# Performance work log

Measured on AMD Instinct MI355X. Metric: run time of the kernel, lower is better.

The kernel has to match this reference:

```python
import jax, jax.numpy as jnp
import numpy as np

G, N, E = 64, 1000, 8192          # graphs, nodes/graph, edges/graph
F_IN, C, H, HID, NCLS = 128, 128, 4, 256, 2
EPS = 1e-5


def _gcn(x, src, dst, W, b):
    # GCNConv: symmetric normalization with self-loops, sum aggregation.
    h = x @ W                                              # [N, C]
    deg = jax.ops.segment_sum(jnp.ones(E, h.dtype), dst, num_segments=N) + 1.0
    dinv = jax.lax.rsqrt(deg)                              # deg^{-1/2}
    msg = h[src] * (dinv[src] * dinv[dst])[:, None]        # [E, C] gather
    out = jax.ops.segment_sum(msg, dst, num_segments=N)    # scatter-add
    out = out + h * (dinv * dinv)[:, None]                 # self-loop term
    return out + b


def _layernorm(y, g, b):
    mu = y.mean(-1, keepdims=True)
    var = ((y - mu) ** 2).mean(-1, keepdims=True)
    return (y - mu) * jax.lax.rsqrt(var + EPS) * g + b


def setup_inputs() -> dict:
    key = jax.random.key(0)
    ks = jax.random.split(key, 12)
    rn = lambda k, s: jax.random.normal(k, s, jnp.float32) * 0.05
    return dict(
        x=jax.random.normal(ks[0], (G, N, F_IN), jnp.float32),
        edge_index=jax.random.randint(ks[1], (G, 2, E), 0, N),
        W0=rn(ks[2], (F_IN, C)), b0=jnp.zeros((C,), jnp.float32),
        W1=rn(ks[3], (C, C)), b1=jnp.zeros((C,), jnp.float32),
        in_w=rn(ks[4], (3 * C, C)), in_b=jnp.zeros((3 * C,), jnp.float32),
        out_w=rn(ks[5], (C, C)), out_b=jnp.zeros((C,), jnp.float32),
        ln2_g=jnp.ones((C,), jnp.float32), ln2_b=jnp.zeros((C,), jnp.float32),
        mw1=rn(ks[6], (C, HID)), mb1=jnp.zeros((HID,), jnp.float32),
        mw2=rn(ks[7], (HID, C)), mb2=jnp.zeros((C,), jnp.float32),
        lw=rn(ks[8], (C, NCLS)), lb=jnp.zeros((NCLS,), jnp.float32),
    )


def reference(x, edge_index, W0, b0, W1, b1, in_w, in_b, out_w, out_b,
              ln2_g, ln2_b, mw1, mb1, mw2, mb2, lw, lb):
    src, dst = edge_index[:, 0, :], edge_index[:, 1, :]
    conv = jax.vmap(_gcn, in_axes=(0, 0, 0, None, None))
    h = jnp.tanh(conv(x, src, dst, W0, b0))   # [G, N, C]
    h = jnp.tanh(conv(h, src, dst, W1, b1))
    g = h.sum(axis=1)                          # SumAggregation -> [G, C]

    # MultiheadAttention, unbatched: sequence of G graph embeddings
    qkv = g @ in_w.T + in_b
    q, k, v = jnp.split(qkv, 3, axis=-1)
    d = C // H
    qh, kh, vh = (t.reshape(G, H, d) for t in (q, k, v))
    attn = jax.nn.softmax(jnp.einsum('qhd,khd->hqk', qh, kh) * (d ** -0.5), axis=-1)
    o = jnp.einsum('hqk,khd->qhd', attn, vh).reshape(G, C) @ out_w.T + out_b

    x_attend = o                               # dropout = identity (eval)
    # NOTE: original computes layer_norm1(x_attend) but immediately overwrites it.
    mlp = jnp.maximum(x_attend @ mw1 + mb1, 0.0) @ mw2 + mb2
    y = _layernorm(x_attend + mlp, ln2_g, ln2_b)
    node_repr = jnp.maximum(y, 0.0).sum(axis=0)  # [C]
    return node_repr @ lw + lb                   # [NCLS]
```

## Files before the change

kernel.cpp:

```cpp
#include <hip/hip_runtime.h>
#include <math.h>

#define Gn 64
#define Nn 1000
#define En 8192
#define Cc 128
#define HIDn 256
#define EPSf 1e-5f

typedef __attribute__((ext_vector_type(8))) short bh8;
typedef __attribute__((ext_vector_type(4))) float fx4;

__device__ __forceinline__ unsigned short f2bf(float f) {
    unsigned u = __float_as_uint(f);
    u += 0x7fffu + ((u >> 16) & 1u);
    return (unsigned short)(u >> 16);
}
__device__ __forceinline__ float bflo(unsigned u) { return __uint_as_float(u << 16); }
__device__ __forceinline__ float bfhi(unsigned u) { return __uint_as_float(u & 0xffff0000u); }

__global__ __launch_bounds__(256) void k_pre(const int* __restrict__ ei,
                                             const float* __restrict__ W0, const float* __restrict__ W1,
                                             int4* __restrict__ ninfo, int2* __restrict__ epair,
                                             float* __restrict__ pooled, float* __restrict__ repr,
                                             int* __restrict__ ctr,
                                             unsigned short* __restrict__ Wt0g,
                                             unsigned short* __restrict__ Wt1g)
{
    __shared__ int   curs[1024];
    __shared__ float dinv_s[1024];
    __shared__ int   wsum[4];
    __shared__ __align__(16) short Wls[128][136];
    int t = threadIdx.x;

    if (blockIdx.x >= 64) {
        const float* Wsrc = (blockIdx.x == 64) ? W0 : W1;
        unsigned short* Wdst = (blockIdx.x == 64) ? Wt0g : Wt1g;
        for (int idx = t; idx < 16384; idx += 256) {
            int kI = idx >> 7, n = idx & 127;
            Wls[n][kI] = (short)f2bf(Wsrc[idx]);
        }
        __syncthreads();
        for (int idx = t; idx < 2048; idx += 256) {
            int n = idx >> 4, kc = idx & 15;
            bh8 v = *(const bh8*)&Wls[n][kc * 8];
            *(bh8*)(Wdst + (size_t)idx * 8) = v;
        }
        return;
    }

    int g = blockIdx.x;
    const int* srcp = ei + (size_t)g * 2 * En;
    const int* dstp = srcp + En;
    int lane = t & 63, wv = t >> 6;

    #pragma unroll
    for (int j = 0; j < 4; ++j) curs[t * 4 + j] = 0;
    __syncthreads();
    for (int e = t; e < En; e += 256) atomicAdd(&curs[dstp[e]], 1);
    __syncthreads();

    int base = t * 4;
    int d0 = curs[base], d1 = curs[base + 1], d2 = curs[base + 2], d3 = curs[base + 3];
    int s = d0 + d1 + d2 + d3;
    int v = s;
    #pragma unroll
    for (int off = 1; off <= 32; off <<= 1) {
        int u = __shfl_up(v, off);
        if (lane >= off) v += u;
    }
    if (lane == 63) wsum[wv] = v;
    __syncthreads();
    int woff = 0;
    #pragma unroll
    for (int w = 0; w < 4; ++w) if (w < wv) woff += wsum[w];
    int e0 = woff + v - s;
    int e1 = e0 + d0, e2 = e1 + d1, e3 = e2 + d2;
    float dv0 = rsqrtf((float)d0 + 1.f), dv1 = rsqrtf((float)d1 + 1.f);
    float dv2 = rsqrtf((float)d2 + 1.f), dv3 = rsqrtf((float)d3 + 1.f);
    curs[base] = e0; curs[base + 1] = e1; curs[base + 2] = e2; curs[base + 3] = e3;
    dinv_s[base] = dv0; dinv_s[base + 1] = dv1; dinv_s[base + 2] = dv2; dinv_s[base + 3] = dv3;
    if (base < Nn)     ninfo[g * Nn + base]     = make_int4(e0, d0, __float_as_int(dv0 * dv0), 0);
    if (base + 1 < Nn) ninfo[g * Nn + base + 1] = make_int4(e1, d1, __float_as_int(dv1 * dv1), 0);
    if (base + 2 < Nn) ninfo[g * Nn + base + 2] = make_int4(e2, d2, __float_as_int(dv2 * dv2), 0);
    if (base + 3 < Nn) ninfo[g * Nn + base + 3] = make_int4(e3, d3, __float_as_int(dv3 * dv3), 0);
    __syncthreads();

    for (int e = t; e < En; e += 256) {
        int dd = dstp[e], ss = srcp[e];
        int p = atomicAdd(&curs[dd], 1);
        float w = dinv_s[ss] * dinv_s[dd];
        epair[(size_t)g * En + p] = make_int2(ss, __float_as_int(w));
    }
    if (t < Cc) pooled[g * Cc + t] = 0.f;
    if (g == 0 && t < Cc) repr[t] = 0.f;
    if (g == 0 && t == 0) *ctr = 0;
}

template<int INBF>
__global__ __launch_bounds__(256) void k_gemm(const void* __restrict__ Xin,
                                              const unsigned short* __restrict__ Wtg,
                                              unsigned short* __restrict__ Hout)
{
    __shared__ __align__(16) short Wt[128][136];
    int b = blockIdx.x;
    int xcd = b & 7, gg = (b >> 3) & 7, rblk = b >> 6;
    int g = xcd + 8 * gg;
    int t = threadIdx.x;
    for (int idx = t; idx < 2048; idx += 256) {
        int n = idx >> 4, kc = idx & 15;
        bh8 v = *(const bh8*)(Wtg + (size_t)idx * 8);
        *(bh8*)&Wt[n][kc * 8] = v;
    }
    __syncthreads();

    int wave = t >> 6, l = t & 63;
    int lr = l & 15, lg = l >> 4;
    const float* Xf = (const float*)Xin + (size_t)g * Nn * Cc;
    const short* Xh = (const short*)Xin + (size_t)g * Nn * Cc;
    unsigned short* Hg = Hout + (size_t)g * Nn * Cc;

    int rbase = rblk * 64 + wave * 16;
    int r = rbase + lr;
    bool ok = r < Nn;
    bh8 af[4];
    if (INBF) {
        #pragma unroll
        for (int ks = 0; ks < 4; ++ks) {
            if (ok) af[ks] = *(const bh8*)(Xh + (size_t)r * Cc + ks * 32 + lg * 8);
            else    af[ks] = bh8{0, 0, 0, 0, 0, 0, 0, 0};
        }
    } else {
        #pragma unroll
        for (int ks = 0; ks < 4; ++ks) {
            if (ok) {
                const float* xp = Xf + (size_t)r * Cc + ks * 32 + lg * 8;
                fx4 a0 = *(const fx4*)xp;
                fx4 a1 = *(const fx4*)(xp + 4);
                bh8 av;
                av[0] = (short)f2bf(a0[0]); av[1] = (short)f2bf(a0[1]);
                av[2] = (short)f2bf(a0[2]); av[3] = (short)f2bf(a0[3]);
                av[4] = (short)f2bf(a1[0]); av[5] = (short)f2bf(a1[1]);
                av[6] = (short)f2bf(a1[2]); av[7] = (short)f2bf(a1[3]);
                af[ks] = av;
            } else af[ks] = bh8{0, 0, 0, 0, 0, 0, 0, 0};
        }
    }
    fx4 acc[8];
    #pragma unroll
    for (int ct = 0; ct < 8; ++ct) acc[ct] = fx4{0.f, 0.f, 0.f, 0.f};
    #pragma unroll
    for (int ks = 0; ks < 4; ++ks) {
        #pragma unroll
        for (int ct = 0; ct < 8; ++ct) {
            bh8 bfr = *(const bh8*)(&Wt[ct * 16 + lr][ks * 32 + lg * 8]);
            acc[ct] = __builtin_amdgcn_mfma_f32_16x16x32_bf16(af[ks], bfr, acc[ct], 0, 0, 0);
        }
    }
    #pragma unroll
    for (int ct = 0; ct < 8; ++ct) {
        #pragma unroll
        for (int rg = 0; rg < 4; ++rg) {
            int row = rbase + lg * 4 + rg;
            if (row < Nn) Hg[(size_t)row * Cc + ct * 16 + lr] = f2bf(acc[ct][rg]);
        }
    }
}

template<int POOL>
__global__ __launch_bounds__(256) void k_combine(const unsigned* __restrict__ Hb, const int2* __restrict__ epair,
                                                 const int4* __restrict__ ninfo, const float* __restrict__ bias,
                                                 unsigned* __restrict__ Tout, float* __restrict__ pooled)
{
    int b = blockIdx.x;
    int xcd = b & 7, j = b >> 3;
    int g = xcd + 8 * (j & 7);
    int blk = j >> 3;
    int wave = threadIdx.x >> 6, lane = threadIdx.x & 63;
    const unsigned* Hg = Hb + (size_t)g * Nn * 64;
    const int2* epg = epair + (size_t)g * En;
    const int4* nig = ninfo + (size_t)g * Nn;
    float2 bb = *(const float2*)(bias + lane * 2);
    float px = 0.f, py = 0.f;
    for (int n = blk * 4 + wave; n < Nn; n += 128) {
        int4 ni = nig[n];
        int st = ni.x, dc = ni.y;
        float sw = __int_as_float(ni.z);
        unsigned hv = Hg[n * 64 + lane];
        float a0x = bflo(hv) * sw + bb.x, a0y = bfhi(hv) * sw + bb.y;
        float a1x = 0.f, a1y = 0.f, a2x = 0.f, a2y = 0.f, a3x = 0.f, a3y = 0.f;
        int e = 0;
        for (; e + 4 <= dc; e += 4) {
            int2 p0 = epg[st + e];
            int2 p1 = epg[st + e + 1];
            int2 p2 = epg[st + e + 2];
            int2 p3 = epg[st + e + 3];
            unsigned r0 = Hg[(size_t)p0.x * 64 + lane];
            unsigned r1 = Hg[(size_t)p1.x * 64 + lane];
            unsigned r2 = Hg[(size_t)p2.x * 64 + lane];
            unsigned r3 = Hg[(size_t)p3.x * 64 + lane];
            float w0 = __int_as_float(p0.y), w1 = __int_as_float(p1.y);
            float w2 = __int_as_float(p2.y), w3 = __int_as_float(p3.y);
            a0x = fmaf(bflo(r0), w0, a0x); a0y = fmaf(bfhi(r0), w0, a0y);
            a1x = fmaf(bflo(r1), w1, a1x); a1y = fmaf(bfhi(r1), w1, a1y);
            a2x = fmaf(bflo(r2), w2, a2x); a2y = fmaf(bfhi(r2), w2, a2y);
            a3x = fmaf(bflo(r3), w3, a3x); a3y = fmaf(bfhi(r3), w3, a3y);
        }
        for (; e < dc; ++e) {
            int2 p0 = epg[st + e];
            unsigned r0 = Hg[(size_t)p0.x * 64 + lane];
            float w0 = __int_as_float(p0.y);
            a0x = fmaf(bflo(r0), w0, a0x); a0y = fmaf(bfhi(r0), w0, a0y);
        }
        float ax = (a0x + a1x) + (a2x + a3x);
        float ay = (a0y + a1y) + (a2y + a3y);
        float tx = tanhf(ax), ty = tanhf(ay);
        if (POOL) { px += tx; py += ty; }
        else Tout[(size_t)(g * Nn + n) * 64 + lane] = ((unsigned)f2bf(ty) << 16) | (unsigned)f2bf(tx);
    }
    if (POOL) {
        atomicAdd(&pooled[g * Cc + lane * 2], px);
        atomicAdd(&pooled[g * Cc + lane * 2 + 1], py);
    }
}

__global__ __launch_bounds__(1024) void k_qkv(const float* __restrict__ pooled, const float* __restrict__ in_w,
                                              const float* __restrict__ in_b, float* __restrict__ qkvb)
{
    int t = threadIdx.x, lane = t & 63, wv = t >> 6;
    int c = blockIdx.x * 16 + wv;
    const float* wr = in_w + c * Cc;
    float w0 = wr[lane], w1 = wr[64 + lane];
    float bias = in_b[c];
    for (int i = 0; i < Gn; ++i) {
        float p = fmaf(pooled[i * Cc + lane], w0, pooled[i * Cc + 64 + lane] * w1);
        #pragma unroll
        for (int off2 = 32; off2 > 0; off2 >>= 1) p += __shfl_xor(p, off2);
        if (lane == 0) qkvb[i * 384 + c] = p + bias;
    }
}

__global__ __launch_bounds__(1024) void k_attn(const float* __restrict__ qkvb, float* __restrict__ ob)
{
    __shared__ float q[64][33], kk[64][33], v[64][33];
    __shared__ float S[64][64];
    int h = blockIdx.x, t = threadIdx.x;

    for (int idx = t; idx < 2048; idx += 1024) {
        int i = idx >> 5, cc = idx & 31;
        q[i][cc]  = qkvb[i * 384 + h * 32 + cc];
        kk[i][cc] = qkvb[i * 384 + 128 + h * 32 + cc];
        v[i][cc]  = qkvb[i * 384 + 256 + h * 32 + cc];
    }
    __syncthreads();

    for (int idx = t; idx < 4096; idx += 1024) {
        int i = idx >> 6, jj = idx & 63;
        float acc = 0.f;
        #pragma unroll
        for (int d2 = 0; d2 < 32; ++d2) acc = fmaf(q[i][d2], kk[jj][d2], acc);
        S[i][jj] = acc * 0.17677669529663687f;
    }
    __syncthreads();

    int lane = t & 63, w = t >> 6;
    for (int r = w; r < 64; r += 16) {
        float val = S[r][lane];
        float m = val;
        #pragma unroll
        for (int off = 32; off > 0; off >>= 1) m = fmaxf(m, __shfl_xor(m, off));
        float e2 = expf(val - m);
        float ssum = e2;
        #pragma unroll
        for (int off = 32; off > 0; off >>= 1) ssum += __shfl_xor(ssum, off);
        S[r][lane] = e2 / ssum;
    }
    __syncthreads();

    for (int idx = t; idx < 2048; idx += 1024) {
        int i = idx >> 5, d2 = idx & 31;
        float acc = 0.f;
        #pragma unroll 4
        for (int k2 = 0; k2 < 64; ++k2) acc = fmaf(S[i][k2], v[k2][d2], acc);
        ob[i * Cc + h * 32 + d2] = acc;
    }
}

__global__ __launch_bounds__(512) void k_tailfinal(const float* __restrict__ ob, const float* __restrict__ out_w,
                                                   const float* __restrict__ out_b, const float* __restrict__ mw1,
                                                   const float* __restrict__ mb1, const float* __restrict__ mw2,
                                                   const float* __restrict__ mb2, const float* __restrict__ ln2g,
                                                   const float* __restrict__ ln2b, const float* __restrict__ lw,
                                                   const float* __restrict__ lb, float* __restrict__ repr,
                                                   int* __restrict__ ctr, float* __restrict__ out)
{
    __shared__ float sob[128];
    __shared__ float sxatt[128];
    __shared__ float sm1p[2][256];
    __shared__ float sm1[256];
    __shared__ float sp2[4][128];
    __shared__ float yb[128];
    __shared__ int slast;
    int g = blockIdx.x;
    int t = threadIdx.x, lane = t & 63, wv = t >> 6;

    if (t < 128) sob[t] = ob[(size_t)g * Cc + t];
    __syncthreads();

    {
        float o0 = sob[lane], o1 = sob[64 + lane];
        for (int c = wv; c < Cc; c += 8) {
            const float* wr = out_w + c * Cc;
            float p = fmaf(o0, wr[lane], o1 * wr[64 + lane]);
            #pragma unroll
            for (int off = 32; off > 0; off >>= 1) p += __shfl_xor(p, off);
            if (lane == 0) sxatt[c] = p + out_b[c];
        }
    }
    __syncthreads();

    {
        int jc = t & 255, half = t >> 8;
        int k0b = half * 64;
        float a[8];
        #pragma unroll
        for (int u = 0; u < 8; ++u) a[u] = 0.f;
        for (int k0 = k0b; k0 < k0b + 64; k0 += 8) {
            #pragma unroll
            for (int u = 0; u < 8; ++u)
                a[u] = fmaf(sxatt[k0 + u], mw1[(size_t)(k0 + u) * HIDn + jc], a[u]);
        }
        sm1p[half][jc] = ((a[0] + a[1]) + (a[2] + a[3])) + ((a[4] + a[5]) + (a[6] + a[7]));
        __syncthreads();
        if (t < 256) sm1[t] = fmaxf(sm1p[0][t] + sm1p[1][t] + mb1[t], 0.f);
    }
    __syncthreads();

    {
        int c = t & 127, q = t >> 7;
        int j0b = q * 64;
        float a[8];
        #pragma unroll
        for (int u = 0; u < 8; ++u) a[u] = 0.f;
        for (int j0 = j0b; j0 < j0b + 64; j0 += 8) {
            #pragma unroll
            for (int u = 0; u < 8; ++u)
                a[u] = fmaf(sm1[j0 + u], mw2[(size_t)(j0 + u) * Cc + c], a[u]);
        }
        sp2[q][c] = ((a[0] + a[1]) + (a[2] + a[3])) + ((a[4] + a[5]) + (a[6] + a[7]));
        __syncthreads();
        if (t < 128) yb[t] = sxatt[t] + (sp2[0][t] + sp2[1][t]) + (sp2[2][t] + sp2[3][t]) + mb2[t];
    }
    __syncthreads();

    if (t < 64) {
        float v0 = yb[lane], v1 = yb[64 + lane];
        float s = v0 + v1;
        #pragma unroll
        for (int off = 32; off > 0; off >>= 1) s += __shfl_xor(s, off);
        float mu = s * (1.f / 128.f);
        float d0 = v0 - mu, d1 = v1 - mu;
        float vv = d0 * d0 + d1 * d1;
        #pragma unroll
        for (int off = 32; off > 0; off >>= 1) vv += __shfl_xor(vv, off);
        float rstd = rsqrtf(vv * (1.f / 128.f) + EPSf);
        float z0 = fmaxf(d0 * rstd * ln2g[lane] + ln2b[lane], 0.f);
        float z1 = fmaxf(d1 * rstd * ln2g[64 + lane] + ln2b[64 + lane], 0.f);
        atomicAdd(&repr[lane], z0);
        atomicAdd(&repr[64 + lane], z1);
    }

    __threadfence();
    __syncthreads();
    if (t == 0) slast = atomicAdd(ctr, 1);
    __syncthreads();
    if (slast == 63) {
        __threadfence();
        __shared__ float r0s[128], r1s[128];
        if (t < 128) {
            float r = __hip_atomic_load(&repr[t], __ATOMIC_RELAXED, __HIP_MEMORY_SCOPE_AGENT);
            r0s[t] = r * lw[t * 2 + 0];
            r1s[t] = r * lw[t * 2 + 1];
        }
        __syncthreads();
        for (int s2 = 64; s2 > 0; s2 >>= 1) {
            if (t < s2) { r0s[t] += r0s[t + s2]; r1s[t] += r1s[t + s2]; }
            __syncthreads();
        }
        if (t == 0) { out[0] = r0s[0] + lb[0]; out[1] = r1s[0] + lb[1]; }
    }
}

extern "C" void kernel_launch(void* const* d_in, const int* in_sizes, int n_in,
                              void* d_out, int out_size, void* d_ws, size_t ws_size,
                              hipStream_t stream)
{
    const float* x     = (const float*)d_in[0];
    const int*   ei    = (const int*)d_in[1];
    const float* W0    = (const float*)d_in[2];
    const float* b0    = (const float*)d_in[3];
    const float* W1    = (const float*)d_in[4];
    const float* b1    = (const float*)d_in[5];
    const float* in_w  = (const float*)d_in[6];
    const float* in_b  = (const float*)d_in[7];
    const float* out_w = (const float*)d_in[8];
    const float* out_b = (const float*)d_in[9];
    const float* ln2g  = (const float*)d_in[10];
    const float* ln2b  = (const float*)d_in[11];
    const float* mw1   = (const float*)d_in[12];
    const float* mb1   = (const float*)d_in[13];
    const float* mw2   = (const float*)d_in[14];
    const float* mb2   = (const float*)d_in[15];
    const float* lw    = (const float*)d_in[16];
    const float* lb    = (const float*)d_in[17];
    float* out = (float*)d_out;
    (void)in_sizes; (void)n_in; (void)out_size; (void)ws_size;

    char* ws = (char*)d_ws;
    size_t off = 0;
    auto carve = [&](size_t bytes) { size_t o = off; off += (bytes + 255) & ~(size_t)255; return o; };
    size_t o_ni    = carve((size_t)Gn * Nn * 16);
    size_t o_ep    = carve((size_t)Gn * En * 8);
    size_t o_pool  = carve((size_t)Gn * Cc * 4);
    size_t o_qkv   = carve((size_t)Gn * 384 * 4);
    size_t o_ob    = carve((size_t)Gn * Cc * 4);
    size_t o_repr  = carve((size_t)Cc * 4);
    size_t o_ctr   = carve(256);
    size_t o_W0t   = carve((size_t)Cc * Cc * 2);
    size_t o_W1t   = carve((size_t)Cc * Cc * 2);
    size_t o_H     = carve((size_t)Gn * Nn * Cc * 2);
    size_t o_T     = carve((size_t)Gn * Nn * Cc * 2);

    int4*  ninfo  = (int4*)(ws + o_ni);
    int2*  epair  = (int2*)(ws + o_ep);
    float* pooled = (float*)(ws + o_pool);
    float* qkvb   = (float*)(ws + o_qkv);
    float* ob     = (float*)(ws + o_ob);
    float* repr   = (float*)(ws + o_repr);
    int*   ctr    = (int*)(ws + o_ctr);
    unsigned short* Wt0g = (unsigned short*)(ws + o_W0t);
    unsigned short* Wt1g = (unsigned short*)(ws + o_W1t);
    unsigned short* H  = (unsigned short*)(ws + o_H);
    unsigned short* T  = (unsigned short*)(ws + o_T);

    k_pre<<<66, 256, 0, stream>>>(ei, W0, W1, ninfo, epair, pooled, repr, ctr, Wt0g, Wt1g);
    k_gemm<0><<<1024, 256, 0, stream>>>(x, Wt0g, H);
    k_combine<0><<<2048, 256, 0, stream>>>((const unsigned*)H, epair, ninfo, b0, (unsigned*)T, nullptr);
    k_gemm<1><<<1024, 256, 0, stream>>>(T, Wt1g, H);
    k_combine<1><<<2048, 256, 0, stream>>>((const unsigned*)H, epair, ninfo, b1, nullptr, pooled);
    k_qkv<<<24, 1024, 0, stream>>>(pooled, in_w, in_b, qkvb);
    k_attn<<<4, 1024, 0, stream>>>(qkvb, ob);
    k_tailfinal<<<64, 512, 0, stream>>>(ob, out_w, out_b, mw1, mb1, mw2, mb2, ln2g, ln2b,
                                        lw, lb, repr, ctr, out);
}
```

Before: 170.4 us.

## Fuse preprocessing with first GEMM and merge attention head kernels via grid barriers

```diff
diff --git a/kernel.cpp b/kernel.cpp
--- a/kernel.cpp
+++ b/kernel.cpp
@@ -19,88 +19,140 @@
 __device__ __forceinline__ float bflo(unsigned u) { return __uint_as_float(u << 16); }
 __device__ __forceinline__ float bfhi(unsigned u) { return __uint_as_float(u & 0xffff0000u); }
 
-__global__ __launch_bounds__(256) void k_pre(const int* __restrict__ ei,
+__global__ __launch_bounds__(256) void k_g0p(const int* __restrict__ ei, const float* __restrict__ X,
                                              const float* __restrict__ W0, const float* __restrict__ W1,
                                              int4* __restrict__ ninfo, int2* __restrict__ epair,
                                              float* __restrict__ pooled, float* __restrict__ repr,
-                                             int* __restrict__ ctr,
-                                             unsigned short* __restrict__ Wt0g,
-                                             unsigned short* __restrict__ Wt1g)
+                                             int* __restrict__ bars,
+                                             unsigned short* __restrict__ Wt1g,
+                                             unsigned short* __restrict__ Hout)
 {
-    __shared__ int   curs[1024];
-    __shared__ float dinv_s[1024];
-    __shared__ int   wsum[4];
-    __shared__ __align__(16) short Wls[128][136];
+    __shared__ __align__(16) short Wt[128][136];
+    __shared__ int wsum[4];
     int t = threadIdx.x;
-
-    if (blockIdx.x >= 64) {
-        const float* Wsrc = (blockIdx.x == 64) ? W0 : W1;
-        unsigned short* Wdst = (blockIdx.x == 64) ? Wt0g : Wt1g;
+    int b = blockIdx.x;
+
+    if (b < 64) {
+        int* curs = (int*)&Wt[0][0];
+        float* dinv_s = (float*)((char*)&Wt[0][0] + 4096);
+        int g = b;
+        const int* srcp = ei + (size_t)g * 2 * En;
+        const int* dstp = srcp + En;
+        int lane = t & 63, wv = t >> 6;
+
+        #pragma unroll
+        for (int j = 0; j < 4; ++j) curs[t * 4 + j] = 0;
+        __syncthreads();
+        for (int e = t; e < En; e += 256) atomicAdd(&curs[dstp[e]], 1);
+        __syncthreads();
+
+        int base = t * 4;
+        int d0 = curs[base], d1 = curs[base + 1], d2 = curs[base + 2], d3 = curs[base + 3];
+        int s = d0 + d1 + d2 + d3;
+        int v = s;
+        #pragma unroll
+        for (int off = 1; off <= 32; off <<= 1) {
+            int u = __shfl_up(v, off);
+            if (lane >= off) v += u;
+        }
+        if (lane == 63) wsum[wv] = v;
+        __syncthreads();
+        int woff = 0;
+        #pragma unroll
+        for (int w = 0; w < 4; ++w) if (w < wv) woff += wsum[w];
+        int e0 = woff + v - s;
+        int e1 = e0 + d0, e2 = e1 + d1, e3 = e2 + d2;
+        float dv0 = rsqrtf((float)d0 + 1.f), dv1 = rsqrtf((float)d1 + 1.f);
+        float dv2 = rsqrtf((float)d2 + 1.f), dv3 = rsqrtf((float)d3 + 1.f);
+        curs[base] = e0; curs[base + 1] = e1; curs[base + 2] = e2; curs[base + 3] = e3;
+        dinv_s[base] = dv0; dinv_s[base + 1] = dv1; dinv_s[base + 2] = dv2; dinv_s[base + 3] = dv3;
+        if (base < Nn)     ninfo[g * Nn + base]     = make_int4(e0, d0, __float_as_int(dv0 * dv0), 0);
+        if (base + 1 < Nn) ninfo[g * Nn + base + 1] = make_int4(e1, d1, __float_as_int(dv1 * dv1), 0);
+        if (base + 2 < Nn) ninfo[g * Nn + base + 2] = make_int4(e2, d2, __float_as_int(dv2 * dv2), 0);
+        if (base + 3 < Nn) ninfo[g * Nn + base + 3] = make_int4(e3, d3, __float_as_int(dv3 * dv3), 0);
+        __syncthreads();
+
+        for (int e = t; e < En; e += 256) {
+            int dd = dstp[e], ss = srcp[e];
+            int p = atomicAdd(&curs[dd], 1);
+            float w = dinv_s[ss] * dinv_s[dd];
+            epair[(size_t)g * En + p] = make_int2(ss, __float_as_int(w));
+        }
+        if (t < Cc) pooled[g * Cc + t] = 0.f;
+        if (g == 0 && t < Cc) repr[t] = 0.f;
+        if (g == 0 && t < 4) bars[t] = 0;
+        return;
+    }
+
+    if (b == 1088) {
         for (int idx = t; idx < 16384; idx += 256) {
             int kI = idx >> 7, n = idx & 127;
-            Wls[n][kI] = (short)f2bf(Wsrc[idx]);
+            Wt[n][kI] = (short)f2bf(W1[idx]);
         }
         __syncthreads();
         for (int idx = t; idx < 2048; idx += 256) {
             int n = idx >> 4, kc = idx & 15;
-            bh8 v = *(const bh8*)&Wls[n][kc * 8];
-            *(bh8*)(Wdst + (size_t)idx * 8) = v;
+            *(bh8*)(Wt1g + (size_t)idx * 8) = *(const bh8*)&Wt[n][kc * 8];
         }
         return;
     }
 
-    int g = blockIdx.x;
-    const int* srcp = ei + (size_t)g * 2 * En;
-    const int* dstp = srcp + En;
-    int lane = t & 63, wv = t >> 6;
-
-    #pragma unroll
-    for (int j = 0; j < 4; ++j) curs[t * 4 + j] = 0;
-    __syncthreads();
-    for (int e = t; e < En; e += 256) atomicAdd(&curs[dstp[e]], 1);
-    __syncthreads();
-
-    int base = t * 4;
-    int d0 = curs[base], d1 = curs[base + 1], d2 = curs[base + 2], d3 = curs[base + 3];
-    int s = d0 + d1 + d2 + d3;
-    int v = s;
-    #pragma unroll
-    for (int off = 1; off <= 32; off <<= 1) {
-        int u = __shfl_up(v, off);
-        if (lane >= off) v += u;
-    }
-    if (lane == 63) wsum[wv] = v;
-    __syncthreads();
-    int woff = 0;
-    #pragma unroll
-    for (int w = 0; w < 4; ++w) if (w < wv) woff += wsum[w];
-    int e0 = woff + v - s;
-    int e1 = e0 + d0, e2 = e1 + d1, e3 = e2 + d2;
-    float dv0 = rsqrtf((float)d0 + 1.f), dv1 = rsqrtf((float)d1 + 1.f);
-    float dv2 = rsqrtf((float)d2 + 1.f), dv3 = rsqrtf((float)d3 + 1.f);
-    curs[base] = e0; curs[base + 1] = e1; curs[base + 2] = e2; curs[base + 3] = e3;
-    dinv_s[base] = dv0; dinv_s[base + 1] = dv1; dinv_s[base + 2] = dv2; dinv_s[base + 3] = dv3;
-    if (base < Nn)     ninfo[g * Nn + base]     = make_int4(e0, d0, __float_as_int(dv0 * dv0), 0);
-    if (base + 1 < Nn) ninfo[g * Nn + base + 1] = make_int4(e1, d1, __float_as_int(dv1 * dv1), 0);
-    if (base + 2 < Nn) ninfo[g * Nn + base + 2] = make_int4(e2, d2, __float_as_int(dv2 * dv2), 0);
-    if (base + 3 < Nn) ninfo[g * Nn + base + 3] = make_int4(e3, d3, __float_as_int(dv3 * dv3), 0);
-    __syncthreads();
-
-    for (int e = t; e < En; e += 256) {
-        int dd = dstp[e], ss = srcp[e];
-        int p = atomicAdd(&curs[dd], 1);
-        float w = dinv_s[ss] * dinv_s[dd];
-        epair[(size_t)g * En + p] = make_int2(ss, __float_as_int(w));
-    }
-    if (t < Cc) pooled[g * Cc + t] = 0.f;
-    if (g == 0 && t < Cc) repr[t] = 0.f;
-    if (g == 0 && t == 0) *ctr = 0;
-}
-
-template<int INBF>
-__global__ __launch_bounds__(256) void k_gemm(const void* __restrict__ Xin,
-                                              const unsigned short* __restrict__ Wtg,
-                                              unsigned short* __restrict__ Hout)
+    int bb = b - 64;
+    int xcd = bb & 7, gg = (bb >> 3) & 7, rblk = bb >> 6;
+    int g = xcd + 8 * gg;
+    for (int idx = t; idx < 16384; idx += 256) {
+        int kI = idx >> 7, n = idx & 127;
+        Wt[n][kI] = (short)f2bf(W0[idx]);
+    }
+    __syncthreads();
+
+    int wave = t >> 6, l = t & 63;
+    int lr = l & 15, lg = l >> 4;
+    const float* Xf = X + (size_t)g * Nn * Cc;
+    unsigned short* Hg = Hout + (size_t)g * Nn * Cc;
+
+    int rbase = rblk * 64 + wave * 16;
+    int r = rbase + lr;
+    bool ok = r < Nn;
+    bh8 af[4];
+    #pragma unroll
+    for (int ks = 0; ks < 4; ++ks) {
+        if (ok) {
+            const float* xp = Xf + (size_t)r * Cc + ks * 32 + lg * 8;
+            fx4 a0 = *(const fx4*)xp;
+            fx4 a1 = *(const fx4*)(xp + 4);
+            bh8 av;
+            av[0] = (short)f2bf(a0[0]); av[1] = (short)f2bf(a0[1]);
+            av[2] = (short)f2bf(a0[2]); av[3] = (short)f2bf(a0[3]);
+            av[4] = (short)f2bf(a1[0]); av[5] = (short)f2bf(a1[1]);
+            av[6] = (short)f2bf(a1[2]); av[7] = (short)f2bf(a1[3]);
+            af[ks] = av;
+        } else af[ks] = bh8{0, 0, 0, 0, 0, 0, 0, 0};
+    }
+    fx4 acc[8];
+    #pragma unroll
+    for (int ct = 0; ct < 8; ++ct) acc[ct] = fx4{0.f, 0.f, 0.f, 0.f};
+    #pragma unroll
+    for (int ks = 0; ks < 4; ++ks) {
+        #pragma unroll
+        for (int ct = 0; ct < 8; ++ct) {
+            bh8 bfr = *(const bh8*)(&Wt[ct * 16 + lr][ks * 32 + lg * 8]);
+            acc[ct] = __builtin_amdgcn_mfma_f32_16x16x32_bf16(af[ks], bfr, acc[ct], 0, 0, 0);
+        }
+    }
+    #pragma unroll
+    for (int ct = 0; ct < 8; ++ct) {
+        #pragma unroll
+        for (int rg = 0; rg < 4; ++rg) {
+            int row = rbase + lg * 4 + rg;
+            if (row < Nn) Hg[(size_t)row * Cc + ct * 16 + lr] = f2bf(acc[ct][rg]);
+        }
+    }
+}
+
+__global__ __launch_bounds__(256) void k_gemm1(const unsigned short* __restrict__ Xh,
+                                               const unsigned short* __restrict__ Wtg,
+                                               unsigned short* __restrict__ Hout)
 {
     __shared__ __align__(16) short Wt[128][136];
     int b = blockIdx.x;
@@ -116,35 +168,17 @@
 
     int wave = t >> 6, l = t & 63;
     int lr = l & 15, lg = l >> 4;
-    const float* Xf = (const float*)Xin + (size_t)g * Nn * Cc;
-    const short* Xh = (const short*)Xin + (size_t)g * Nn * Cc;
+    const short* Xg = (const short*)Xh + (size_t)g * Nn * Cc;
     unsigned short* Hg = Hout + (size_t)g * Nn * Cc;
 
     int rbase = rblk * 64 + wave * 16;
     int r = rbase + lr;
     bool ok = r < Nn;
     bh8 af[4];
-    if (INBF) {
-        #pragma unroll
-        for (int ks = 0; ks < 4; ++ks) {
-            if (ok) af[ks] = *(const bh8*)(Xh + (size_t)r * Cc + ks * 32 + lg * 8);
-            else    af[ks] = bh8{0, 0, 0, 0, 0, 0, 0, 0};
-        }
-    } else {
-        #pragma unroll
-        for (int ks = 0; ks < 4; ++ks) {
-            if (ok) {
-                const float* xp = Xf + (size_t)r * Cc + ks * 32 + lg * 8;
-                fx4 a0 = *(const fx4*)xp;
-                fx4 a1 = *(const fx4*)(xp + 4);
-                bh8 av;
-                av[0] = (short)f2bf(a0[0]); av[1] = (short)f2bf(a0[1]);
-                av[2] = (short)f2bf(a0[2]); av[3] = (short)f2bf(a0[3]);
-                av[4] = (short)f2bf(a1[0]); av[5] = (short)f2bf(a1[1]);
-                av[6] = (short)f2bf(a1[2]); av[7] = (short)f2bf(a1[3]);
-                af[ks] = av;
-            } else af[ks] = bh8{0, 0, 0, 0, 0, 0, 0, 0};
-        }
+    #pragma unroll
+    for (int ks = 0; ks < 4; ++ks) {
+        if (ok) af[ks] = *(const bh8*)(Xg + (size_t)r * Cc + ks * 32 + lg * 8);
+        else    af[ks] = bh8{0, 0, 0, 0, 0, 0, 0, 0};
     }
     fx4 acc[8];
     #pragma unroll
@@ -186,7 +220,7 @@
         int4 ni = nig[n];
         int st = ni.x, dc = ni.y;
         float sw = __int_as_float(ni.z);
-        unsigned hv = Hg[n * 64 + lane];
+        unsigned hv = Hg[(size_t)n * 64 + lane];
         float a0x = bflo(hv) * sw + bb.x, a0y = bfhi(hv) * sw + bb.y;
         float a1x = 0.f, a1y = 0.f, a2x = 0.f, a2y = 0.f, a3x = 0.f, a3y = 0.f;
         int e = 0;
@@ -224,87 +258,94 @@
     }
 }
 
-__global__ __launch_bounds__(1024) void k_qkv(const float* __restrict__ pooled, const float* __restrict__ in_w,
-                                              const float* __restrict__ in_b, float* __restrict__ qkvb)
+__global__ __launch_bounds__(512) void k_head(const float* __restrict__ pooled, const float* __restrict__ in_w,
+                                              const float* __restrict__ in_b, const float* __restrict__ out_w,
+                                              const float* __restrict__ out_b, const float* __restrict__ mw1,
+                                              const float* __restrict__ mb1, const float* __restrict__ mw2,
+                                              const float* __restrict__ mb2, const float* __restrict__ ln2g,
+                                              const float* __restrict__ ln2b, const float* __restrict__ lw,
+                                              const float* __restrict__ lb, float* __restrict__ qkvb,
+                                              float* __restrict__ ob, float* __restrict__ repr,
+                                              int* __restrict__ bars, float* __restrict__ out)
 {
-    int t = threadIdx.x, lane = t & 63, wv = t >> 6;
-    int c = blockIdx.x * 16 + wv;
-    const float* wr = in_w + c * Cc;
-    float w0 = wr[lane], w1 = wr[64 + lane];
-    float bias = in_b[c];
-    for (int i = 0; i < Gn; ++i) {
-        float p = fmaf(pooled[i * Cc + lane], w0, pooled[i * Cc + 64 + lane] * w1);
-        #pragma unroll
-        for (int off2 = 32; off2 > 0; off2 >>= 1) p += __shfl_xor(p, off2);
-        if (lane == 0) qkvb[i * 384 + c] = p + bias;
-    }
-}
-
-__global__ __launch_bounds__(1024) void k_attn(const float* __restrict__ qkvb, float* __restrict__ ob)
-{
-    __shared__ float q[64][33], kk[64][33], v[64][33];
+    __shared__ float spool[128];
+    __shared__ float q[64][33], kk[64][33], vv[64][33];
     __shared__ float S[64][64];
-    int h = blockIdx.x, t = threadIdx.x;
-
-    for (int idx = t; idx < 2048; idx += 1024) {
-        int i = idx >> 5, cc = idx & 31;
-        q[i][cc]  = qkvb[i * 384 + h * 32 + cc];
-        kk[i][cc] = qkvb[i * 384 + 128 + h * 32 + cc];
-        v[i][cc]  = qkvb[i * 384 + 256 + h * 32 + cc];
-    }
-    __syncthreads();
-
-    for (int idx = t; idx < 4096; idx += 1024) {
-        int i = idx >> 6, jj = idx & 63;
-        float acc = 0.f;
-        #pragma unroll
-        for (int d2 = 0; d2 < 32; ++d2) acc = fmaf(q[i][d2], kk[jj][d2], acc);
-        S[i][jj] = acc * 0.17677669529663687f;
-    }
-    __syncthreads();
-
-    int lane = t & 63, w = t >> 6;
-    for (int r = w; r < 64; r += 16) {
-        float val = S[r][lane];
-        float m = val;
-        #pragma unroll
-        for (int off = 32; off > 0; off >>= 1) m = fmaxf(m, __shfl_xor(m, off));
-        float e2 = expf(val - m);
-        float ssum = e2;
-        #pragma unroll
-        for (int off = 32; off > 0; off >>= 1) ssum += __shfl_xor(ssum, off);
-        S[r][lane] = e2 / ssum;
-    }
-    __syncthreads();
-
-    for (int idx = t; idx < 2048; idx += 1024) {
-        int i = idx >> 5, d2 = idx & 31;
-        float acc = 0.f;
-        #pragma unroll 4
-        for (int k2 = 0; k2 < 64; ++k2) acc = fmaf(S[i][k2], v[k2][d2], acc);
-        ob[i * Cc + h * 32 + d2] = acc;
-    }
-}
-
-__global__ __launch_bounds__(512) void k_tailfinal(const float* __restrict__ ob, const float* __restrict__ out_w,
-                                                   const float* __restrict__ out_b, const float* __restrict__ mw1,
-                                                   const float* __restrict__ mb1, const float* __restrict__ mw2,
-                                                   const float* __restrict__ mb2, const float* __restrict__ ln2g,
-                                                   const float* __restrict__ ln2b, const float* __restrict__ lw,
-                                                   const float* __restrict__ lb, float* __restrict__ repr,
-                                                   int* __restrict__ ctr, float* __restrict__ out)
-{
-    __shared__ float sob[128];
-    __shared__ float sxatt[128];
-    __shared__ float sm1p[2][256];
-    __shared__ float sm1[256];
-    __shared__ float sp2[4][128];
-    __shared__ float yb[128];
+    __shared__ float sob[128], sxatt[128], sm1p[2][256], sm1[256], sp2[4][128], yb[128];
     __shared__ int slast;
-    int g = blockIdx.x;
-    int t = threadIdx.x, lane = t & 63, wv = t >> 6;
-
-    if (t < 128) sob[t] = ob[(size_t)g * Cc + t];
+    int g = blockIdx.x, t = threadIdx.x, lane = t & 63, wv = t >> 6;
+
+    if (t < 128) spool[t] = pooled[g * Cc + t];
+    __syncthreads();
+    {
+        float p0 = spool[lane], p1 = spool[64 + lane];
+        for (int c = wv; c < 384; c += 8) {
+            const float* wr = in_w + c * Cc;
+            float p = fmaf(p0, wr[lane], p1 * wr[64 + lane]);
+            #pragma unroll
+            for (int off = 32; off > 0; off >>= 1) p += __shfl_xor(p, off);
+            if (lane == 0)
+                __hip_atomic_store(&qkvb[g * 384 + c], p + in_b[c],
+                                   __ATOMIC_RELAXED, __HIP_MEMORY_SCOPE_AGENT);
+        }
+    }
+    __syncthreads();
+    if (t == 0) {
+        __hip_atomic_fetch_add(&bars[0], 1, __ATOMIC_RELEASE, __HIP_MEMORY_SCOPE_AGENT);
+        while (__hip_atomic_load(&bars[0], __ATOMIC_ACQUIRE, __HIP_MEMORY_SCOPE_AGENT) < Gn) {}
+    }
+    __syncthreads();
+
+    if (g < 4) {
+        int h = g;
+        for (int idx = t; idx < 2048; idx += 512) {
+            int i = idx >> 5, cc = idx & 31;
+            q[i][cc]  = __hip_atomic_load(&qkvb[i * 384 + h * 32 + cc],
+                                          __ATOMIC_RELAXED, __HIP_MEMORY_SCOPE_AGENT);
+            kk[i][cc] = __hip_atomic_load(&qkvb[i * 384 + 128 + h * 32 + cc],
+                                          __ATOMIC_RELAXED, __HIP_MEMORY_SCOPE_AGENT);
+            vv[i][cc] = __hip_atomic_load(&qkvb[i * 384 + 256 + h * 32 + cc],
+                                          __ATOMIC_RELAXED, __HIP_MEMORY_SCOPE_AGENT);
+        }
+        __syncthreads();
+        for (int idx = t; idx < 4096; idx += 512) {
+            int i = idx >> 6, jj = idx & 63;
+            float acc = 0.f;
+            #pragma unroll
+            for (int d2 = 0; d2 < 32; ++d2) acc = fmaf(q[i][d2], kk[jj][d2], acc);
+            S[i][jj] = acc * 0.17677669529663687f;
+        }
+        __syncthreads();
+        for (int r = wv; r < 64; r += 8) {
+            float val = S[r][lane];
+            float m = val;
+            #pragma unroll
+            for (int off = 32; off > 0; off >>= 1) m = fmaxf(m, __shfl_xor(m, off));
+            float e2 = expf(val - m);
+            float ssum = e2;
+            #pragma unroll
+            for (int off = 32; off > 0; off >>= 1) ssum += __shfl_xor(ssum, off);
+            S[r][lane] = e2 / ssum;
+        }
+        __syncthreads();
+        for (int idx = t; idx < 2048; idx += 512) {
+            int i = idx >> 5, d2 = idx & 31;
+            float acc = 0.f;
+            #pragma unroll 4
+            for (int k2 = 0; k2 < 64; ++k2) acc = fmaf(S[i][k2], vv[k2][d2], acc);
+            __hip_atomic_store(&ob[i * Cc + h * 32 + d2], acc,
+                               __ATOMIC_RELAXED, __HIP_MEMORY_SCOPE_AGENT);
+        }
+    }
+    __syncthreads();
+    if (t == 0) {
+        __hip_atomic_fetch_add(&bars[1], 1, __ATOMIC_RELEASE, __HIP_MEMORY_SCOPE_AGENT);
+        while (__hip_atomic_load(&bars[1], __ATOMIC_ACQUIRE, __HIP_MEMORY_SCOPE_AGENT) < Gn) {}
+    }
+    __syncthreads();
+
+    if (t < 128) sob[t] = __hip_atomic_load(&ob[(size_t)g * Cc + t],
+                                            __ATOMIC_RELAXED, __HIP_MEMORY_SCOPE_AGENT);
     __syncthreads();
 
     {
@@ -337,8 +378,8 @@
     __syncthreads();
 
     {
-        int c = t & 127, q = t >> 7;
-        int j0b = q * 64;
+        int c = t & 127, qq = t >> 7;
+        int j0b = qq * 64;
         float a[8];
         #pragma unroll
         for (int u = 0; u < 8; ++u) a[u] = 0.f;
@@ -347,7 +388,7 @@
             for (int u = 0; u < 8; ++u)
                 a[u] = fmaf(sm1[j0 + u], mw2[(size_t)(j0 + u) * Cc + c], a[u]);
         }
-        sp2[q][c] = ((a[0] + a[1]) + (a[2] + a[3])) + ((a[4] + a[5]) + (a[6] + a[7]));
+        sp2[qq][c] = ((a[0] + a[1]) + (a[2] + a[3])) + ((a[4] + a[5]) + (a[6] + a[7]));
         __syncthreads();
         if (t < 128) yb[t] = sxatt[t] + (sp2[0][t] + sp2[1][t]) + (sp2[2][t] + sp2[3][t]) + mb2[t];
     }
@@ -360,10 +401,10 @@
         for (int off = 32; off > 0; off >>= 1) s += __shfl_xor(s, off);
         float mu = s * (1.f / 128.f);
         float d0 = v0 - mu, d1 = v1 - mu;
-        float vv = d0 * d0 + d1 * d1;
-        #pragma unroll
-        for (int off = 32; off > 0; off >>= 1) vv += __shfl_xor(vv, off);
-        float rstd = rsqrtf(vv * (1.f / 128.f) + EPSf);
+        float vvr = d0 * d0 + d1 * d1;
+        #pragma unroll
+        for (int off = 32; off > 0; off >>= 1) vvr += __shfl_xor(vvr, off);
+        float rstd = rsqrtf(vvr * (1.f / 128.f) + EPSf);
         float z0 = fmaxf(d0 * rstd * ln2g[lane] + ln2b[lane], 0.f);
         float z1 = fmaxf(d1 * rstd * ln2g[64 + lane] + ln2b[64 + lane], 0.f);
         atomicAdd(&repr[lane], z0);
@@ -372,7 +413,7 @@
 
     __threadfence();
     __syncthreads();
-    if (t == 0) slast = atomicAdd(ctr, 1);
+    if (t == 0) slast = atomicAdd(&bars[2], 1);
     __syncthreads();
     if (slast == 63) {
         __threadfence();
@@ -425,8 +466,7 @@
     size_t o_qkv   = carve((size_t)Gn * 384 * 4);
     size_t o_ob    = carve((size_t)Gn * Cc * 4);
     size_t o_repr  = carve((size_t)Cc * 4);
-    size_t o_ctr   = carve(256);
-    size_t o_W0t   = carve((size_t)Cc * Cc * 2);
+    size_t o_bars  = carve(256);
     size_t o_W1t   = carve((size_t)Cc * Cc * 2);
     size_t o_H     = carve((size_t)Gn * Nn * Cc * 2);
     size_t o_T     = carve((size_t)Gn * Nn * Cc * 2);
@@ -437,19 +477,15 @@
     float* qkvb   = (float*)(ws + o_qkv);
     float* ob     = (float*)(ws + o_ob);
     float* repr   = (float*)(ws + o_repr);
-    int*   ctr    = (int*)(ws + o_ctr);
-    unsigned short* Wt0g = (unsigned short*)(ws + o_W0t);
+    int*   bars   = (int*)(ws + o_bars);
     unsigned short* Wt1g = (unsigned short*)(ws + o_W1t);
     unsigned short* H  = (unsigned short*)(ws + o_H);
     unsigned short* T  = (unsigned short*)(ws + o_T);
 
-    k_pre<<<66, 256, 0, stream>>>(ei, W0, W1, ninfo, epair, pooled, repr, ctr, Wt0g, Wt1g);
-    k_gemm<0><<<1024, 256, 0, stream>>>(x, Wt0g, H);
+    k_g0p<<<1089, 256, 0, stream>>>(ei, x, W0, W1, ninfo, epair, pooled, repr, bars, Wt1g, H);
     k_combine<0><<<2048, 256, 0, stream>>>((const unsigned*)H, epair, ninfo, b0, (unsigned*)T, nullptr);
-    k_gemm<1><<<1024, 256, 0, stream>>>(T, Wt1g, H);
+    k_gemm1<<<1024, 256, 0, stream>>>(T, Wt1g, H);
     k_combine<1><<<2048, 256, 0, stream>>>((const unsigned*)H, epair, ninfo, b1, nullptr, pooled);
-    k_qkv<<<24, 1024, 0, stream>>>(pooled, in_w, in_b, qkvb);
-    k_attn<<<4, 1024, 0, stream>>>(qkvb, ob);
-    k_tailfinal<<<64, 512, 0, stream>>>(ob, out_w, out_b, mw1, mb1, mw2, mb2, ln2g, ln2b,
-                                        lw, lb, repr, ctr, out);
-}
+    k_head<<<64, 512, 0, stream>>>(pooled, in_w, in_b, out_w, out_b, mw1, mb1, mw2, mb2,
+                                   ln2g, ln2b, lw, lb, qkvb, ob, repr, bars, out);
+}
```

After: 176.3 us. 1.03x slower.

## Fuse graph preprocessing and first-layer GEMM into a single kernel launch

Applied to the files above, without the earlier changes.

```diff
diff --git a/kernel.cpp b/kernel.cpp
--- a/kernel.cpp
+++ b/kernel.cpp
@@ -19,88 +19,140 @@
 __device__ __forceinline__ float bflo(unsigned u) { return __uint_as_float(u << 16); }
 __device__ __forceinline__ float bfhi(unsigned u) { return __uint_as_float(u & 0xffff0000u); }
 
-__global__ __launch_bounds__(256) void k_pre(const int* __restrict__ ei,
+__global__ __launch_bounds__(256) void k_g0p(const int* __restrict__ ei, const float* __restrict__ X,
                                              const float* __restrict__ W0, const float* __restrict__ W1,
                                              int4* __restrict__ ninfo, int2* __restrict__ epair,
                                              float* __restrict__ pooled, float* __restrict__ repr,
-                                             int* __restrict__ ctr,
-                                             unsigned short* __restrict__ Wt0g,
-                                             unsigned short* __restrict__ Wt1g)
-{
-    __shared__ int   curs[1024];
-    __shared__ float dinv_s[1024];
-    __shared__ int   wsum[4];
-    __shared__ __align__(16) short Wls[128][136];
+                                             int* __restrict__ bars,
+                                             unsigned short* __restrict__ Wt1g,
+                                             unsigned short* __restrict__ Hout)
+{
+    __shared__ __align__(16) short Wt[128][136];
+    __shared__ int wsum[4];
     int t = threadIdx.x;
-
-    if (blockIdx.x >= 64) {
-        const float* Wsrc = (blockIdx.x == 64) ? W0 : W1;
-        unsigned short* Wdst = (blockIdx.x == 64) ? Wt0g : Wt1g;
+    int b = blockIdx.x;
+
+    if (b < 64) {
+        int* curs = (int*)&Wt[0][0];
+        float* dinv_s = (float*)((char*)&Wt[0][0] + 4096);
+        int g = b;
+        const int* srcp = ei + (size_t)g * 2 * En;
+        const int* dstp = srcp + En;
+        int lane = t & 63, wv = t >> 6;
+
+        #pragma unroll
+        for (int j = 0; j < 4; ++j) curs[t * 4 + j] = 0;
+        __syncthreads();
+        for (int e = t; e < En; e += 256) atomicAdd(&curs[dstp[e]], 1);
+        __syncthreads();
+
+        int base = t * 4;
+        int d0 = curs[base], d1 = curs[base + 1], d2 = curs[base + 2], d3 = curs[base + 3];
+        int s = d0 + d1 + d2 + d3;
+        int v = s;
+        #pragma unroll
+        for (int off = 1; off <= 32; off <<= 1) {
+            int u = __shfl_up(v, off);
+            if (lane >= off) v += u;
+        }
+        if (lane == 63) wsum[wv] = v;
+        __syncthreads();
+        int woff = 0;
+        #pragma unroll
+        for (int w = 0; w < 4; ++w) if (w < wv) woff += wsum[w];
+        int e0 = woff + v - s;
+        int e1 = e0 + d0, e2 = e1 + d1, e3 = e2 + d2;
+        float dv0 = rsqrtf((float)d0 + 1.f), dv1 = rsqrtf((float)d1 + 1.f);
+        float dv2 = rsqrtf((float)d2 + 1.f), dv3 = rsqrtf((float)d3 + 1.f);
+        curs[base] = e0; curs[base + 1] = e1; curs[base + 2] = e2; curs[base + 3] = e3;
+        dinv_s[base] = dv0; dinv_s[base + 1] = dv1; dinv_s[base + 2] = dv2; dinv_s[base + 3] = dv3;
+        if (base < Nn)     ninfo[g * Nn + base]     = make_int4(e0, d0, __float_as_int(dv0 * dv0), 0);
+        if (base + 1 < Nn) ninfo[g * Nn + base + 1] = make_int4(e1, d1, __float_as_int(dv1 * dv1), 0);
+        if (base + 2 < Nn) ninfo[g * Nn + base + 2] = make_int4(e2, d2, __float_as_int(dv2 * dv2), 0);
+        if (base + 3 < Nn) ninfo[g * Nn + base + 3] = make_int4(e3, d3, __float_as_int(dv3 * dv3), 0);
+        __syncthreads();
+
+        for (int e = t; e < En; e += 256) {
+            int dd = dstp[e], ss = srcp[e];
+            int p = atomicAdd(&curs[dd], 1);
+            float w = dinv_s[ss] * dinv_s[dd];
+            epair[(size_t)g * En + p] = make_int2(ss, __float_as_int(w));
+        }
+        if (t < Cc) pooled[g * Cc + t] = 0.f;
+        if (g == 0 && t < Cc) repr[t] = 0.f;
+        if (g == 0 && t < 4) bars[t] = 0;
+        return;
+    }
+
+    if (b == 1088) {
         for (int idx = t; idx < 16384; idx += 256) {
             int kI = idx >> 7, n = idx & 127;
-            Wls[n][kI] = (short)f2bf(Wsrc[idx]);
+            Wt[n][kI] = (short)f2bf(W1[idx]);
         }
         __syncthreads();
         for (int idx = t; idx < 2048; idx += 256) {
             int n = idx >> 4, kc = idx & 15;
-            bh8 v = *(const bh8*)&Wls[n][kc * 8];
-            *(bh8*)(Wdst + (size_t)idx * 8) = v;
+            *(bh8*)(Wt1g + (size_t)idx * 8) = *(const bh8*)&Wt[n][kc * 8];
         }
         return;
     }
 
-    int g = blockIdx.x;
-    const int* srcp = ei + (size_t)g * 2 * En;
-    const int* dstp = srcp + En;
-    int lane = t & 63, wv = t >> 6;
-
-    #pragma unroll
-    for (int j = 0; j < 4; ++j) curs[t * 4 + j] = 0;
-    __syncthreads();
-    for (int e = t; e < En; e += 256) atomicAdd(&curs[dstp[e]], 1);
-    __syncthreads();
-
-    int base = t * 4;
-    int d0 = curs[base], d1 = curs[base + 1], d2 = curs[base + 2], d3 = curs[base + 3];
-    int s = d0 + d1 + d2 + d3;
-    int v = s;
-    #pragma unroll
-    for (int off = 1; off <= 32; off <<= 1) {
-        int u = __shfl_up(v, off);
-        if (lane >= off) v += u;
-    }
-    if (lane == 63) wsum[wv] = v;
-    __syncthreads();
-    int woff = 0;
-    #pragma unroll
-    for (int w = 0; w < 4; ++w) if (w < wv) woff += wsum[w];
-    int e0 = woff + v - s;
-    int e1 = e0 + d0, e2 = e1 + d1, e3 = e2 + d2;
-    float dv0 = rsqrtf((float)d0 + 1.f), dv1 = rsqrtf((float)d1 + 1.f);
-    float dv2 = rsqrtf((float)d2 + 1.f), dv3 = rsqrtf((float)d3 + 1.f);
-    curs[base] = e0; curs[base + 1] = e1; curs[base + 2] = e2; curs[base + 3] = e3;
-    dinv_s[base] = dv0; dinv_s[base + 1] = dv1; dinv_s[base + 2] = dv2; dinv_s[base + 3] = dv3;
-    if (base < Nn)     ninfo[g * Nn + base]     = make_int4(e0, d0, __float_as_int(dv0 * dv0), 0);
-    if (base + 1 < Nn) ninfo[g * Nn + base + 1] = make_int4(e1, d1, __float_as_int(dv1 * dv1), 0);
-    if (base + 2 < Nn) ninfo[g * Nn + base + 2] = make_int4(e2, d2, __float_as_int(dv2 * dv2), 0);
-    if (base + 3 < Nn) ninfo[g * Nn + base + 3] = make_int4(e3, d3, __float_as_int(dv3 * dv3), 0);
-    __syncthreads();
-
-    for (int e = t; e < En; e += 256) {
-        int dd = dstp[e], ss = srcp[e];
-        int p = atomicAdd(&curs[dd], 1);
-        float w = dinv_s[ss] * dinv_s[dd];
-        epair[(size_t)g * En + p] = make_int2(ss, __float_as_int(w));
-    }
-    if (t < Cc) pooled[g * Cc + t] = 0.f;
-    if (g == 0 && t < Cc) repr[t] = 0.f;
-    if (g == 0 && t == 0) *ctr = 0;
-}
-
-template<int INBF>
-__global__ __launch_bounds__(256) void k_gemm(const void* __restrict__ Xin,
-                                              const unsigned short* __restrict__ Wtg,
-                                              unsigned short* __restrict__ Hout)
+    int bb = b - 64;
+    int xcd = bb & 7, gg = (bb >> 3) & 7, rblk = bb >> 6;
+    int g = xcd + 8 * gg;
+    for (int idx = t; idx < 16384; idx += 256) {
+        int kI = idx >> 7, n = idx & 127;
+        Wt[n][kI] = (short)f2bf(W0[idx]);
+    }
+    __syncthreads();
+
+    int wave = t >> 6, l = t & 63;
+    int lr = l & 15, lg = l >> 4;
+    const float* Xf = X + (size_t)g * Nn * Cc;
+    unsigned short* Hg = Hout + (size_t)g * Nn * Cc;
+
+    int rbase = rblk * 64 + wave * 16;
+    int r = rbase + lr;
+    bool ok = r < Nn;
+    bh8 af[4];
+    #pragma unroll
+    for (int ks = 0; ks < 4; ++ks) {
+        if (ok) {
+            const float* xp = Xf + (size_t)r * Cc + ks * 32 + lg * 8;
+            fx4 a0 = *(const fx4*)xp;
+            fx4 a1 = *(const fx4*)(xp + 4);
+            bh8 av;
+            av[0] = (short)f2bf(a0[0]); av[1] = (short)f2bf(a0[1]);
+            av[2] = (short)f2bf(a0[2]); av[3] = (short)f2bf(a0[3]);
+            av[4] = (short)f2bf(a1[0]); av[5] = (short)f2bf(a1[1]);
+            av[6] = (short)f2bf(a1[2]); av[7] = (short)f2bf(a1[3]);
+            af[ks] = av;
+        } else af[ks] = bh8{0, 0, 0, 0, 0, 0, 0, 0};
+    }
+    fx4 acc[8];
+    #pragma unroll
+    for (int ct = 0; ct < 8; ++ct) acc[ct] = fx4{0.f, 0.f, 0.f, 0.f};
+    #pragma unroll
+    for (int ks = 0; ks < 4; ++ks) {
+        #pragma unroll
+        for (int ct = 0; ct < 8; ++ct) {
+            bh8 bfr = *(const bh8*)(&Wt[ct * 16 + lr][ks * 32 + lg * 8]);
+            acc[ct] = __builtin_amdgcn_mfma_f32_16x16x32_bf16(af[ks], bfr, acc[ct], 0, 0, 0);
+        }
+    }
+    #pragma unroll
+    for (int ct = 0; ct < 8; ++ct) {
+        #pragma unroll
+        for (int rg = 0; rg < 4; ++rg) {
+            int row = rbase + lg * 4 + rg;
+            if (row < Nn) Hg[(size_t)row * Cc + ct * 16 + lr] = f2bf(acc[ct][rg]);
+        }
+    }
+}
+
+__global__ __launch_bounds__(256) void k_gemm1(const unsigned short* __restrict__ Xh,
+                                               const unsigned short* __restrict__ Wtg,
+                                               unsigned short* __restrict__ Hout)
 {
     __shared__ __align__(16) short Wt[128][136];
     int b = blockIdx.x;
@@ -116,35 +168,17 @@
 
     int wave = t >> 6, l = t & 63;
     int lr = l & 15, lg = l >> 4;
-    const float* Xf = (const float*)Xin + (size_t)g * Nn * Cc;
-    const short* Xh = (const short*)Xin + (size_t)g * Nn * Cc;
+    const short* Xg = (const short*)Xh + (size_t)g * Nn * Cc;
     unsigned short* Hg = Hout + (size_t)g * Nn * Cc;
 
     int rbase = rblk * 64 + wave * 16;
     int r = rbase + lr;
     bool ok = r < Nn;
     bh8 af[4];
-    if (INBF) {
-        #pragma unroll
-        for (int ks = 0; ks < 4; ++ks) {
-            if (ok) af[ks] = *(const bh8*)(Xh + (size_t)r * Cc + ks * 32 + lg * 8);
-            else    af[ks] = bh8{0, 0, 0, 0, 0, 0, 0, 0};
-        }
-    } else {
-        #pragma unroll
-        for (int ks = 0; ks < 4; ++ks) {
-            if (ok) {
-                const float* xp = Xf + (size_t)r * Cc + ks * 32 + lg * 8;
-                fx4 a0 = *(const fx4*)xp;
-                fx4 a1 = *(const fx4*)(xp + 4);
-                bh8 av;
-                av[0] = (short)f2bf(a0[0]); av[1] = (short)f2bf(a0[1]);
-                av[2] = (short)f2bf(a0[2]); av[3] = (short)f2bf(a0[3]);
-                av[4] = (short)f2bf(a1[0]); av[5] = (short)f2bf(a1[1]);
-                av[6] = (short)f2bf(a1[2]); av[7] = (short)f2bf(a1[3]);
-                af[ks] = av;
-            } else af[ks] = bh8{0, 0, 0, 0, 0, 0, 0, 0};
-        }
+    #pragma unroll
+    for (int ks = 0; ks < 4; ++ks) {
+        if (ok) af[ks] = *(const bh8*)(Xg + (size_t)r * Cc + ks * 32 + lg * 8);
+        else    af[ks] = bh8{0, 0, 0, 0, 0, 0, 0, 0};
     }
     fx4 acc[8];
     #pragma unroll
@@ -186,7 +220,7 @@
         int4 ni = nig[n];
         int st = ni.x, dc = ni.y;
         float sw = __int_as_float(ni.z);
-        unsigned hv = Hg[n * 64 + lane];
+        unsigned hv = Hg[(size_t)n * 64 + lane];
         float a0x = bflo(hv) * sw + bb.x, a0y = bfhi(hv) * sw + bb.y;
         float a1x = 0.f, a1y = 0.f, a2x = 0.f, a2y = 0.f, a3x = 0.f, a3y = 0.f;
         int e = 0;
@@ -425,8 +459,7 @@
     size_t o_qkv   = carve((size_t)Gn * 384 * 4);
     size_t o_ob    = carve((size_t)Gn * Cc * 4);
     size_t o_repr  = carve((size_t)Cc * 4);
-    size_t o_ctr   = carve(256);
-    size_t o_W0t   = carve((size_t)Cc * Cc * 2);
+    size_t o_bars  = carve(256);
     size_t o_W1t   = carve((size_t)Cc * Cc * 2);
     size_t o_H     = carve((size_t)Gn * Nn * Cc * 2);
     size_t o_T     = carve((size_t)Gn * Nn * Cc * 2);
@@ -437,19 +470,17 @@
     float* qkvb   = (float*)(ws + o_qkv);
     float* ob     = (float*)(ws + o_ob);
     float* repr   = (float*)(ws + o_repr);
-    int*   ctr    = (int*)(ws + o_ctr);
-    unsigned short* Wt0g = (unsigned short*)(ws + o_W0t);
+    int*   bars   = (int*)(ws + o_bars);
     unsigned short* Wt1g = (unsigned short*)(ws + o_W1t);
     unsigned short* H  = (unsigned short*)(ws + o_H);
     unsigned short* T  = (unsigned short*)(ws + o_T);
 
-    k_pre<<<66, 256, 0, stream>>>(ei, W0, W1, ninfo, epair, pooled, repr, ctr, Wt0g, Wt1g);
-    k_gemm<0><<<1024, 256, 0, stream>>>(x, Wt0g, H);
+    k_g0p<<<1089, 256, 0, stream>>>(ei, x, W0, W1, ninfo, epair, pooled, repr, bars, Wt1g, H);
     k_combine<0><<<2048, 256, 0, stream>>>((const unsigned*)H, epair, ninfo, b0, (unsigned*)T, nullptr);
-    k_gemm<1><<<1024, 256, 0, stream>>>(T, Wt1g, H);
+    k_gemm1<<<1024, 256, 0, stream>>>(T, Wt1g, H);
     k_combine<1><<<2048, 256, 0, stream>>>((const unsigned*)H, epair, ninfo, b1, nullptr, pooled);
     k_qkv<<<24, 1024, 0, stream>>>(pooled, in_w, in_b, qkvb);
     k_attn<<<4, 1024, 0, stream>>>(qkvb, ob);
     k_tailfinal<<<64, 512, 0, stream>>>(ob, out_w, out_b, mw1, mb1, mw2, mb2, ln2g, ln2b,
-                                        lw, lb, repr, ctr, out);
-}
+                                        lw, lb, repr, &bars[2], out);
+}
```

Result: faster. 159.7 us (-6.3%).
